# Kernel tuning notes

Hardware: AMD Instinct MI355X
Metric: run time of the kernel (lower is better)

The kernel has to match this reference:

```python
import jax, jax.numpy as jnp
import numpy as np

TEMP = 0.5
NUM_QUERIES = 256
NUM_NEGATIVES = 256
STRONG_THRESHOLD = 0.97


def _l2norm(x):
    n = jnp.sqrt(jnp.sum(x * x, axis=-1, keepdims=True))
    return x / jnp.maximum(n, 1e-12)


def _mls(mu0, mu1, s0, s1, w0, w1):
    # mutual likelihood score, mean over feature dim
    mu0 = _l2norm(mu0)
    mu1 = _l2norm(mu1)
    up = (mu0 * w0 - mu1 * w1) ** 2
    down = s0 * w0 + s1 * w1
    return -0.5 * jnp.mean(up / down + jnp.log(down), axis=-1)


def setup_inputs() -> dict:
    key = jax.random.key(0)
    B, C, H, W, S = 4, 32, 256, 256, 8
    ks = jax.random.split(key, 6)
    weights = jax.random.uniform(ks[0], (B, C, H, W), jnp.float32, 0.1, 1.0)
    mu = jax.random.normal(ks[1], (B, C, H, W), jnp.float32)
    sigma = jax.random.uniform(ks[2], (B, C, H, W), jnp.float32, 0.1, 1.0)
    cls = jax.random.randint(ks[3], (B, H, W), 0, S)
    label = jax.nn.one_hot(cls, S, axis=1, dtype=jnp.float32)  # [B,S,H,W]
    mask = (jax.random.uniform(ks[4], (B, 1, H, W)) < 0.7).astype(jnp.float32)
    prob = jax.random.uniform(ks[5], (B, S, H, W), jnp.float32)
    return {"weights": weights, "mu": mu, "sigma": sigma, "label": label, "mask": mask, "prob": prob}


def _rank_table(m, N):
    # m: bool [S, N]. table[s, r] = pixel index with rank r within class s.
    S = m.shape[0]
    ranks = jnp.cumsum(m, axis=1) - 1
    idx = jnp.where(m, ranks, N)  # out-of-range entries are dropped
    tbl = jnp.zeros((S, N), jnp.int32)
    rows = jnp.broadcast_to(jnp.arange(S)[:, None], (S, N))
    vals = jnp.broadcast_to(jnp.arange(N, dtype=jnp.int32)[None, :], (S, N))
    return tbl.at[rows, idx].set(vals, mode="drop")


def _forward(weights, mu, sigma, label, mask, prob):
    B, C, H, W = mu.shape
    S = label.shape[1]
    N = B * H * W
    Q, NEG = NUM_QUERIES, NUM_NEGATIVES
    mu_f = jnp.transpose(mu, (0, 2, 3, 1)).reshape(N, C)
    sig_f = jnp.transpose(sigma, (0, 2, 3, 1)).reshape(N, C)
    w_f = jnp.transpose(weights, (0, 2, 3, 1)).reshape(N, C)
    valid = jnp.transpose(label * mask, (1, 0, 2, 3)).reshape(S, N)  # [S,N]
    prob_f = jnp.transpose(prob, (1, 0, 2, 3)).reshape(S, N)
    vmask = valid > 0
    hmask = vmask & (prob_f < STRONG_THRESHOLD)
    count = jnp.sum(vmask, axis=1)
    hcount = jnp.sum(hmask, axis=1)
    # prototypes: masked sums over valid pixels (no_grad in original)
    inv_sig_w = w_f / sig_f
    proto_sigma = 1.0 / (valid @ inv_sig_w)                    # [S,C]
    proto_mu = proto_sigma * (valid @ (inv_sig_w * mu_f))      # [S,C]
    proto_weight = 1.0 / (valid @ (1.0 / w_f))                 # [S,C]
    proto_mu, proto_sigma, proto_weight = map(jax.lax.stop_gradient, (proto_mu, proto_sigma, proto_weight))
    tbl_valid = _rank_table(vmask, N)
    tbl_hard = _rank_table(hmask, N)
    keys = jax.random.split(jax.random.key(42), S)

    def per_class(i, key):
        k1, k2, k3 = jax.random.split(key, 3)
        # anchor sampling from hard pixels of class i (differentiable gather)
        ra = jnp.minimum((jax.random.uniform(k1, (Q,)) * hcount[i]).astype(jnp.int32), jnp.maximum(hcount[i] - 1, 0))
        apix = tbl_hard[i, ra]
        a_mu, a_sig, a_w = mu_f[apix], sig_f[apix], w_f[apix]
        # negative class distribution from prototype similarity
        order = (i + 1 + jnp.arange(S - 1)) % S
        sim = _mls(proto_mu[i][None], proto_mu[order], proto_sigma[i][None], proto_sigma[order], proto_weight[i][None], proto_weight[order])
        sim = jnp.where(count[order] > 0, sim, -jnp.inf)
        cls_pick = jax.random.categorical(k2, sim / TEMP, shape=(Q, NEG))
        neg_cls = order[cls_pick]                              # [Q,NEG]
        cnt = count[neg_cls]
        rn = jnp.minimum((jax.random.uniform(k3, (Q, NEG)) * cnt).astype(jnp.int32), jnp.maximum(cnt - 1, 0))
        npix = tbl_valid[neg_cls, rn]                          # [Q,NEG]
        n_mu = jax.lax.stop_gradient(mu_f[npix])
        n_sig = jax.lax.stop_gradient(sig_f[npix])
        n_w = jax.lax.stop_gradient(w_f[npix])
        pos_mu = jnp.broadcast_to(proto_mu[i], (Q, 1, C))
        pos_sig = jnp.broadcast_to(proto_sigma[i], (Q, 1, C))
        pos_w = jnp.broadcast_to(proto_weight[i], (Q, 1, C))
        all_mu = jnp.concatenate([pos_mu, n_mu], axis=1)       # [Q,1+NEG,C]
        all_sig = jnp.concatenate([pos_sig, n_sig], axis=1)
        all_w = jnp.concatenate([pos_w, n_w], axis=1)
        logits = _mls(a_mu[:, None], all_mu, a_sig[:, None], all_sig, a_w[:, None], all_w) / TEMP
        ce = jnp.mean(jax.nn.logsumexp(logits, axis=1) - logits[:, 0])
        ok = (hcount[i] > 0) & (count[i] > 0)
        return jnp.where(ok, ce, 0.0)

    losses = jax.vmap(per_class)(jnp.arange(S), keys)
    valid_num = jnp.sum(count > 0)
    return jnp.sum(losses) / valid_num.astype(losses.dtype)


def reference(weights, mu, sigma, label, mask, prob):
    return _forward(weights, mu, sigma, label, mask, prob)
```

## Files before the change

### kernel.cpp

```cpp
#include <hip/hip_runtime.h>
#include <hip/hip_fp16.h>
#include <stdint.h>


#define NPIX  262144
#define NCLS  8
#define NQ    256
#define NNEG  256
#define NE    257
#define NBLK  1024

typedef unsigned short u16;
typedef unsigned int   u32;

struct TFKeys { u32 k1[8][2], k2[8][2], k3[8][2]; };

__host__ __device__ inline void tf2x32(u32 k0, u32 k1, u32 x0, u32 x1, u32& o0, u32& o1) {
  u32 ks2 = k0 ^ k1 ^ 0x1BD11BDAu;
  x0 += k0; x1 += k1;
#define TFR(R) { x0 += x1; x1 = (x1 << (R)) | (x1 >> (32 - (R))); x1 ^= x0; }
  TFR(13) TFR(15) TFR(26) TFR(6)
  x0 += k1;  x1 += ks2 + 1u;
  TFR(17) TFR(29) TFR(16) TFR(24)
  x0 += ks2; x1 += k0 + 2u;
  TFR(13) TFR(15) TFR(26) TFR(6)
  x0 += k0;  x1 += k1 + 3u;
  TFR(17) TFR(29) TFR(16) TFR(24)
  x0 += k1;  x1 += ks2 + 4u;
  TFR(13) TFR(15) TFR(26) TFR(6)
  x0 += ks2; x1 += k0 + 5u;
#undef TFR
  o0 = x0; o1 = x1;
}

__device__ inline float bfv(u16 v) { return __uint_as_float(((u32)v) << 16); }
__device__ inline float lo16(u32 v) { return __uint_as_float(v << 16); }
__device__ inline float hi16(u32 v) { return __uint_as_float(v & 0xFFFF0000u); }
__device__ inline float u01(u32 bits) { return __uint_as_float((bits >> 9) | 0x3F800000u) - 1.0f; }
__device__ inline u32 rbits(u32 k0, u32 k1, u32 idx) { u32 a, b; tf2x32(k0, k1, 0u, idx, a, b); return a ^ b; }
__device__ inline u32 packPQ(float p, float q) {
  return (u32)__half_as_ushort(__float2half(p)) | ((u32)__half_as_ushort(__float2half(q)) << 16);
}
__device__ inline float2 unpackPQ(u32 v) {
  return make_float2(__half2float(__ushort_as_half((u16)(v & 0xFFFFu))),
                     __half2float(__ushort_as_half((u16)(v >> 16))));
}

__global__ __launch_bounds__(256) void k_flags(const u16* __restrict__ lab, const u16* __restrict__ msk,
                                               const u16* __restrict__ prb, unsigned char* __restrict__ flags,
                                               int* __restrict__ blockCnt,
                                               float* __restrict__ protoAcc, float* __restrict__ ceAcc,
                                               int* __restrict__ diag) {
  __shared__ int cnt[16];
  int tid = threadIdx.x;
  if (blockIdx.x == 0) {
    for (int i = tid; i < 768; i += 256) protoAcc[i] = 0.f;
    if (tid < 8) ceAcc[tid] = 0.f;
    if (tid == 0) diag[0] = 0;
  }
  if (tid < 16) cnt[tid] = 0;
  __syncthreads();
  int n = blockIdx.x * 256 + tid;
  int b = n >> 16, hw = n & 65535;
  float m = bfv(msk[(b << 16) + hw]);
  int cls = 0; bool v = false;
  for (int s = 0; s < 8; s++) {
    float l = bfv(lab[((size_t)(b * 8 + s) << 16) + hw]);
    if (l * m > 0.f) { cls = s; v = true; }
  }
  bool h = false;
  if (v) { float p = bfv(prb[((size_t)(b * 8 + cls) << 16) + hw]); h = p < 0.97f; }
  flags[n] = (unsigned char)(cls | (v ? 16 : 0) | (h ? 32 : 0));
  if (v) atomicAdd(&cnt[cls], 1);
  if (h) atomicAdd(&cnt[8 + cls], 1);
  __syncthreads();
  if (tid < 16) blockCnt[tid * NBLK + blockIdx.x] = cnt[tid];
}

__global__ __launch_bounds__(1024) void k_scan(const int* __restrict__ blockCnt, int* __restrict__ blockOff,
                                               int* __restrict__ counts) {
  int ctr = threadIdx.x >> 6, lane = threadIdx.x & 63;
  int run = 0;
  for (int ch = 0; ch < 16; ch++) {
    int bidx = ch * 64 + lane;
    int v = blockCnt[ctr * NBLK + bidx];
    int x = v;
    for (int d = 1; d < 64; d <<= 1) { int t = __shfl_up(x, d); if (lane >= d) x += t; }
    blockOff[ctr * NBLK + bidx] = run + x - v;
    run += __shfl(x, 63);
  }
  if (lane == 0) counts[ctr] = run;
}

__global__ __launch_bounds__(256) void k_place(const unsigned char* __restrict__ flags, const int* __restrict__ blockOff,
                                               int* __restrict__ tblV, int* __restrict__ tblH) {
  __shared__ int wcnt[4][16];
  int tid = threadIdx.x;
  int n = blockIdx.x * 256 + tid;
  int f = flags[n];
  int cls = f & 15; bool v = (f & 16) != 0, h = (f & 32) != 0;
  int wave = tid >> 6, lane = tid & 63;
  unsigned long long below = (1ull << lane) - 1ull;
  int rv = 0, rh = 0;
  for (int s = 0; s < 8; s++) {
    unsigned long long bv = __ballot(v && (cls == s));
    unsigned long long bh = __ballot(h && (cls == s));
    if (lane == 0) { wcnt[wave][s] = __popcll(bv); wcnt[wave][8 + s] = __popcll(bh); }
    if (cls == s) { rv = __popcll(bv & below); rh = __popcll(bh & below); }
  }
  __syncthreads();
  int preV = 0, preH = 0;
  for (int w2 = 0; w2 < wave; w2++) { preV += wcnt[w2][cls]; preH += wcnt[w2][8 + cls]; }
  if (v) tblV[(size_t)cls * NPIX + blockOff[cls * NBLK + blockIdx.x] + preV + rv] = n;
  if (h) tblH[(size_t)cls * NPIX + blockOff[(8 + cls) * NBLK + blockIdx.x] + preH + rh] = n;
}

__global__ __launch_bounds__(256) void k_pq(const u16* __restrict__ mu, const u16* __restrict__ wgt,
                                            const u16* __restrict__ sig, u32* __restrict__ PQ) {
  __shared__ u32 tile[256 * 33];
  int t = threadIdx.x;
  int n0 = blockIdx.x * 512;
  int b = n0 >> 16;
  int hwt = (n0 & 65535) + 2 * t;
  size_t cb = ((size_t)(b * 32)) << 16;
  u32 m2[32];
  float ss0 = 0.f, ss1 = 0.f;
  #pragma unroll
  for (int c = 0; c < 32; c++) {
    m2[c] = *(const u32*)(mu + cb + ((size_t)c << 16) + hwt);
    float a = lo16(m2[c]), d = hi16(m2[c]);
    ss0 += a * a; ss1 += d * d;
  }
  float rn0 = 1.0f / fmaxf(sqrtf(ss0), 1e-12f);
  float rn1 = 1.0f / fmaxf(sqrtf(ss1), 1e-12f);
  u32 pk0[32], pk1[32];
  #pragma unroll
  for (int c = 0; c < 32; c++) {
    u32 w2 = *(const u32*)(wgt + cb + ((size_t)c << 16) + hwt);
    u32 s2 = *(const u32*)(sig + cb + ((size_t)c << 16) + hwt);
    pk0[c] = packPQ(lo16(m2[c]) * rn0 * lo16(w2), lo16(s2) * lo16(w2));
    pk1[c] = packPQ(hi16(m2[c]) * rn1 * hi16(w2), hi16(s2) * hi16(w2));
  }
  #pragma unroll
  for (int ch = 0; ch < 2; ch++) {
    if ((t >> 7) == ch) {
      int l = t & 127;
      #pragma unroll
      for (int c = 0; c < 32; c++) {
        tile[(2 * l + 0) * 33 + c] = pk0[c];
        tile[(2 * l + 1) * 33 + c] = pk1[c];
      }
    }
    __syncthreads();
    uint4* dst = (uint4*)(PQ + (size_t)(n0 + ch * 256) * 32);
    for (int k = t; k < 2048; k += 256) {
      int p = k >> 3, c4 = (k & 7) * 4;
      dst[k] = make_uint4(tile[p * 33 + c4], tile[p * 33 + c4 + 1],
                          tile[p * 33 + c4 + 2], tile[p * 33 + c4 + 3]);
    }
    __syncthreads();
  }
}

__global__ __launch_bounds__(256) void k_proto(const u16* __restrict__ mu, const u16* __restrict__ wgt,
                                               const u16* __restrict__ sig, const int* __restrict__ tblV,
                                               const int* __restrict__ counts, float* __restrict__ protoAcc) {
  int ch = blockIdx.x & 7;
  int s  = (blockIdx.x >> 3) & 7;
  int c  = blockIdx.x >> 6;
  int sc = s * 32 + c;
  int cnt = counts[s];
  const int* row = tblV + (size_t)s * NPIX;
  float a0 = 0.f, a1 = 0.f, a2 = 0.f;
  int r = ch * 256 + threadIdx.x;
  for (; r + 6144 < cnt; r += 8192) {
    int p0 = row[r], p1 = row[r + 2048], p2 = row[r + 4096], p3 = row[r + 6144];
    size_t A0 = (((size_t)((p0 >> 16) * 32 + c)) << 16) + (p0 & 65535);
    size_t A1 = (((size_t)((p1 >> 16) * 32 + c)) << 16) + (p1 & 65535);
    size_t A2 = (((size_t)((p2 >> 16) * 32 + c)) << 16) + (p2 & 65535);
    size_t A3 = (((size_t)((p3 >> 16) * 32 + c)) << 16) + (p3 & 65535);
    float m0 = bfv(mu[A0]), w0 = bfv(wgt[A0]), s0 = bfv(sig[A0]);
    float m1 = bfv(mu[A1]), w1 = bfv(wgt[A1]), s1 = bfv(sig[A1]);
    float m2_ = bfv(mu[A2]), w2 = bfv(wgt[A2]), s2 = bfv(sig[A2]);
    float m3 = bfv(mu[A3]), w3 = bfv(wgt[A3]), s3 = bfv(sig[A3]);
    float i0 = w0 / s0, i1 = w1 / s1, i2 = w2 / s2, i3 = w3 / s3;
    a0 += i0; a1 += i0 * m0; a2 += 1.0f / w0;
    a0 += i1; a1 += i1 * m1; a2 += 1.0f / w1;
    a0 += i2; a1 += i2 * m2_; a2 += 1.0f / w2;
    a0 += i3; a1 += i3 * m3; a2 += 1.0f / w3;
  }
  for (; r < cnt; r += 2048) {
    int pix = row[r];
    size_t a = (((size_t)((pix >> 16) * 32 + c)) << 16) + (pix & 65535);
    float mv = bfv(mu[a]), wv = bfv(wgt[a]), sv = bfv(sig[a]);
    float isw = wv / sv;
    a0 += isw; a1 += isw * mv; a2 += 1.0f / wv;
  }
  #pragma unroll
  for (int d = 1; d < 64; d <<= 1) {
    a0 += __shfl_xor(a0, d);
    a1 += __shfl_xor(a1, d);
    a2 += __shfl_xor(a2, d);
  }
  if ((threadIdx.x & 63) == 0) {
    atomicAdd(&protoAcc[sc * 3 + 0], a0);
    atomicAdd(&protoAcc[sc * 3 + 1], a1);
    atomicAdd(&protoAcc[sc * 3 + 2], a2);
  }
}

__global__ void k_protoFinal(const float* __restrict__ protoAcc, const int* __restrict__ counts,
                             u32* __restrict__ protoPQ, float* __restrict__ simL,
                             int* __restrict__ diag) {
  __shared__ float sP[256], sQ[256];
  __shared__ int alive;
  int tid = threadIdx.x;
  if (tid == 0) alive = 0;
  float a0 = protoAcc[tid * 3 + 0], a1 = protoAcc[tid * 3 + 1], a2 = protoAcc[tid * 3 + 2];
  bool have = counts[tid >> 5] > 0;
  bool ok = (a0 > 0.f) && (a2 > 0.f);
  __syncthreads();
  if (have && !ok) atomicOr(diag, 2);
  if (have && ok) alive = 1;
  float psig = 1.0f / a0;
  float pmu  = psig * a1;
  float pw   = 1.0f / a2;
  float sq = (have && ok) ? pmu * pmu : 0.f;
  #pragma unroll
  for (int d = 1; d < 32; d <<= 1) sq += __shfl_xor(sq, d);
  float rn = 1.0f / fmaxf(sqrtf(sq), 1e-12f);
  float pP = (have && ok) ? pmu * rn * pw : 0.f;
  float pQ = (have && ok) ? psig * pw : 0.f;
  sP[tid] = pP; sQ[tid] = pQ;
  protoPQ[tid] = packPQ(pP, pQ);
  __syncthreads();
  if (tid == 0 && alive == 0) atomicOr(diag, 32);
  if (tid < 64) {
    int i = tid >> 3, j = tid & 7;
    if (j < 7) {
      int o = (i + 1 + j) & 7;
      float acc = 0.f;
      for (int c = 0; c < 32; c++) {
        float d = sP[i * 32 + c] - sP[o * 32 + c];
        float dn = sQ[i * 32 + c] + sQ[o * 32 + c];
        acc += d * d / dn + logf(dn);
      }
      float sim = -0.5f * (acc * (1.0f / 32.0f));
      simL[i * 8 + j] = (counts[o] > 0) ? (sim * 2.0f) : -INFINITY;
    }
  }
}

__global__ __launch_bounds__(256) void k_sample(TFKeys K, const float* __restrict__ simL,
                                                const int* __restrict__ counts,
                                                const int* __restrict__ tblV, const int* __restrict__ tblH,
                                                const u32* __restrict__ PQ, const u32* __restrict__ protoPQ,
                                                float* __restrict__ ceAcc, int* __restrict__ diag) {
  __shared__ __align__(16) u32 sA[32];
  __shared__ float redM[4], redS[4];
  __shared__ int sAp;
  int blk = blockIdx.x;
  int i = blk >> 8, q = blk & 255;
  int t = threadIdx.x;
  if (t == 0) {
    u32 bits = rbits(K.k1[i][0], K.k1[i][1], (u32)q);
    float u = u01(bits);
    int hc = counts[8 + i];
    int ra = (int)(u * (float)hc);
    int cap = hc - 1; if (cap < 0) cap = 0;
    if (ra > cap) ra = cap; if (ra < 0) ra = 0;
    int p = tblH[(size_t)i * NPIX + ra];
    if (p < 0) p = 0; if (p > NPIX - 1) p = NPIX - 1;
    sAp = p;
  }
  __syncthreads();
  if (t < 32) sA[t] = PQ[(size_t)sAp * 32 + t];
  u32 rem = (u32)(q * 256 + t);
  u32 k20 = K.k2[i][0], k21 = K.k2[i][1];
  float Lr[7];
  #pragma unroll
  for (int j = 0; j < 7; j++) Lr[j] = simL[i * 8 + j];
  float mg = 0.f; int pick = 0;
  #pragma unroll
  for (int j = 0; j < 7; j++) {
    u32 bits = rbits(k20, k21, rem * 7u + (u32)j);
    float f = u01(bits);
    float u = fmaxf(f, 1.17549435e-38f);
    float g = -logf(-logf(u));
    float v = g + Lr[j];
    if (j == 0) { mg = v; } else if (v > mg) { mg = v; pick = j; }
  }
  int nc = (i + 1 + pick) & 7;
  u32 bits3 = rbits(K.k3[i][0], K.k3[i][1], rem);
  float u3 = u01(bits3);
  int cntv = counts[nc];
  int rn = (int)(u3 * (float)cntv);
  int cap2 = cntv - 1; if (cap2 < 0) cap2 = 0;
  if (rn > cap2) rn = cap2; if (rn < 0) rn = 0;
  int np = tblV[(size_t)nc * NPIX + rn];
  if (np < 0) np = 0; if (np > NPIX - 1) np = NPIX - 1;
  __syncthreads();
  const uint4* A4 = (const uint4*)sA;
  const uint4* B  = (const uint4*)(PQ + (size_t)np * 32);
  float accN = 0.f;
  #pragma unroll
  for (int k = 0; k < 8; k++) {
    uint4 ua = A4[k], ub = B[k];
    float2 fa, fb; float d, dn;
    fa = unpackPQ(ua.x); fb = unpackPQ(ub.x); d = fa.x - fb.x; dn = fa.y + fb.y; accN += d * d / dn + __logf(dn);
    fa = unpackPQ(ua.y); fb = unpackPQ(ub.y); d = fa.x - fb.x; dn = fa.y + fb.y; accN += d * d / dn + __logf(dn);
    fa = unpackPQ(ua.z); fb = unpackPQ(ub.z); d = fa.x - fb.x; dn = fa.y + fb.y; accN += d * d / dn + __logf(dn);
    fa = unpackPQ(ua.w); fb = unpackPQ(ub.w); d = fa.x - fb.x; dn = fa.y + fb.y; accN += d * d / dn + __logf(dn);
  }
  float lN = -(accN * (1.0f / 32.0f));
  float l0 = 0.f;
  if (t == 0) {
    const uint4* B0 = (const uint4*)(protoPQ + i * 32);
    float acc0 = 0.f;
    #pragma unroll
    for (int k = 0; k < 8; k++) {
      uint4 ua = A4[k], ub = B0[k];
      float2 fa, fb; float d, dn;
      fa = unpackPQ(ua.x); fb = unpackPQ(ub.x); d = fa.x - fb.x; dn = fa.y + fb.y; acc0 += d * d / dn + __logf(dn);
      fa = unpackPQ(ua.y); fb = unpackPQ(ub.y); d = fa.x - fb.x; dn = fa.y + fb.y; acc0 += d * d / dn + __logf(dn);
      fa = unpackPQ(ua.z); fb = unpackPQ(ub.z); d = fa.x - fb.x; dn = fa.y + fb.y; acc0 += d * d / dn + __logf(dn);
      fa = unpackPQ(ua.w); fb = unpackPQ(ub.w); d = fa.x - fb.x; dn = fa.y + fb.y; acc0 += d * d / dn + __logf(dn);
    }
    l0 = -(acc0 * (1.0f / 32.0f));
  }
  bool bad = !(lN == lN) || (t == 0 && !(l0 == l0));
  if (__ballot(bad) != 0ull && (t & 63) == 0) atomicOr(diag, 8);
  float lm = (t == 0) ? fmaxf(lN, l0) : lN;
  #pragma unroll
  for (int d = 1; d < 64; d <<= 1) lm = fmaxf(lm, __shfl_xor(lm, d));
  if ((t & 63) == 0) redM[t >> 6] = lm;
  __syncthreads();
  float M = fmaxf(fmaxf(redM[0], redM[1]), fmaxf(redM[2], redM[3]));
  float es = __expf(lN - M) + ((t == 0) ? __expf(l0 - M) : 0.f);
  #pragma unroll
  for (int d = 1; d < 64; d <<= 1) es += __shfl_xor(es, d);
  if ((t & 63) == 0) redS[t >> 6] = es;
  __syncthreads();
  if (t == 0) {
    float S = redS[0] + redS[1] + redS[2] + redS[3];
    float ce = (M + __logf(S)) - l0;
    atomicAdd(&ceAcc[i], ce);
  }
}

__global__ void k_final(const float* __restrict__ ceAcc, const int* __restrict__ counts,
                        const int* __restrict__ diag, u32* __restrict__ out) {
  if (blockIdx.x == 0 && threadIdx.x == 0) {
    float loss = 0.f; int vn = 0;
    int db = diag[0];
    for (int i = 0; i < 8; i++) {
      if (counts[i] > 0) vn++;
      float ce = ceAcc[i];
      if (counts[i] > 0 && counts[8 + i] > 0) {
        if (!(ce == ce)) db |= 4;
        loss += ce * (1.0f / 256.0f);
      }
    }
    if (vn == 0) db |= 1;
    loss = loss / (float)vn;
    if (!(loss == loss) && db == 0) db = 16;
    if (db != 0) loss = 4096.0f * (float)(1 + db);
    u32 fb = __float_as_uint(loss);
    u32 bv = (fb + 0x7FFFu + ((fb >> 16) & 1u)) >> 16;
    out[0] = (fb & 0xFFFF0000u) | (bv & 0xFFFFu);
  }
}

extern "C" void kernel_launch(void* const* d_in, const int* in_sizes, int n_in,
                              void* d_out, int out_size, void* d_ws, size_t ws_size,
                              hipStream_t stream) {
  (void)in_sizes; (void)n_in; (void)out_size; (void)ws_size;
  const u16* wgt = (const u16*)d_in[0];
  const u16* mu  = (const u16*)d_in[1];
  const u16* sig = (const u16*)d_in[2];
  const u16* lab = (const u16*)d_in[3];
  const u16* msk = (const u16*)d_in[4];
  const u16* prb = (const u16*)d_in[5];

  char* wp = (char*)d_ws;
  auto take = [&](size_t bytes) -> void* { void* p = (void*)wp; wp += ((bytes + 255) & ~(size_t)255); return p; };
  u32*   PQ       = (u32*)  take((size_t)NPIX * 32 * 4);
  int*   tblV     = (int*)  take((size_t)NCLS * NPIX * 4);
  int*   tblH     = (int*)  take((size_t)NCLS * NPIX * 4);
  unsigned char* flags = (unsigned char*)take(NPIX);
  int*   blockCnt = (int*)  take(16 * NBLK * 4);
  int*   blockOff = (int*)  take(16 * NBLK * 4);
  float* protoAcc = (float*)take(768 * 4);
  u32*   protoPQ  = (u32*)  take(256 * 4);
  float* simL     = (float*)take(64 * 4);
  int*   counts   = (int*)  take(16 * 4);
  float* ceAcc    = (float*)take(8 * 4);
  int*   diag     = (int*)  take(4);

  TFKeys K;
  for (u32 i = 0; i < 8; i++) {
    u32 ki0, ki1;
    tf2x32(0u, 42u, 0u, i, ki0, ki1);
    tf2x32(ki0, ki1, 0u, 0u, K.k1[i][0], K.k1[i][1]);
    tf2x32(ki0, ki1, 0u, 1u, K.k2[i][0], K.k2[i][1]);
    tf2x32(ki0, ki1, 0u, 2u, K.k3[i][0], K.k3[i][1]);
  }

  k_flags<<<1024, 256, 0, stream>>>(lab, msk, prb, flags, blockCnt, protoAcc, ceAcc, diag);
  k_scan<<<1, 1024, 0, stream>>>(blockCnt, blockOff, counts);
  k_place<<<1024, 256, 0, stream>>>(flags, blockOff, tblV, tblH);
  k_pq<<<512, 256, 0, stream>>>(mu, wgt, sig, PQ);
  k_proto<<<2048, 256, 0, stream>>>(mu, wgt, sig, tblV, counts, protoAcc);
  k_protoFinal<<<1, 256, 0, stream>>>(protoAcc, counts, protoPQ, simL, diag);
  k_sample<<<2048, 256, 0, stream>>>(K, simL, counts, tblV, tblH, PQ, protoPQ, ceAcc, diag);
  k_final<<<1, 64, 0, stream>>>(ceAcc, counts, diag, (u32*)d_out);
}
```

Measured before the change: 232.5 us.

## Fold scan, protoFinal and final kernels into neighbors via last-block counters

Removes three tiny single-block launches by merging the block-count scan into an extra block of k_pq, and the prototype finalization and loss reduction into the last finishing block of k_proto and k_sample via atomic counters. k_flags now processes four pixels per thread with vectorized loads, emitting four sub-block counts per block. The MLS inner loop replaces per-element log with products of denominators and two logs, plus fast division, cutting transcendental work. Risks: the product of 16 denominators could overflow or underflow, and the scan block in k_pq sits at the tail of the grid.

```diff
diff --git a/kernel.cpp b/kernel.cpp
--- a/kernel.cpp
+++ b/kernel.cpp
@@ -7,7 +7,6 @@
 #define NCLS  8
 #define NQ    256
 #define NNEG  256
-#define NE    257
 #define NBLK  1024
 
 typedef unsigned short u16;
@@ -45,51 +44,119 @@
   return make_float2(__half2float(__ushort_as_half((u16)(v & 0xFFFFu))),
                      __half2float(__ushort_as_half((u16)(v >> 16))));
 }
+__device__ inline float aload(const float* p) {
+  return __hip_atomic_load(p, __ATOMIC_RELAXED, __HIP_MEMORY_SCOPE_AGENT);
+}
 
 __global__ __launch_bounds__(256) void k_flags(const u16* __restrict__ lab, const u16* __restrict__ msk,
                                                const u16* __restrict__ prb, unsigned char* __restrict__ flags,
                                                int* __restrict__ blockCnt,
                                                float* __restrict__ protoAcc, float* __restrict__ ceAcc,
-                                               int* __restrict__ diag) {
-  __shared__ int cnt[16];
-  int tid = threadIdx.x;
+                                               int* __restrict__ diag, int* __restrict__ syncCtr) {
+  __shared__ int cnt[4][16];
+  int t = threadIdx.x;
   if (blockIdx.x == 0) {
-    for (int i = tid; i < 768; i += 256) protoAcc[i] = 0.f;
-    if (tid < 8) ceAcc[tid] = 0.f;
-    if (tid == 0) diag[0] = 0;
-  }
-  if (tid < 16) cnt[tid] = 0;
-  __syncthreads();
-  int n = blockIdx.x * 256 + tid;
-  int b = n >> 16, hw = n & 65535;
-  float m = bfv(msk[(b << 16) + hw]);
-  int cls = 0; bool v = false;
+    for (int i = t; i < 768; i += 256) protoAcc[i] = 0.f;
+    if (t < 8) ceAcc[t] = 0.f;
+    if (t == 0) { diag[0] = 0; syncCtr[0] = 0; syncCtr[1] = 0; }
+  }
+  if (t < 64) cnt[t >> 4][t & 15] = 0;
+  __syncthreads();
+  int n0 = blockIdx.x * 1024;
+  int b = n0 >> 16;
+  int hwt = (n0 & 65535) + 4 * t;
+  uint2 mr = *(const uint2*)(msk + ((size_t)b << 16) + hwt);
+  float m[4] = { lo16(mr.x), hi16(mr.x), lo16(mr.y), hi16(mr.y) };
+  int cls[4] = {0, 0, 0, 0};
+  bool v[4] = {false, false, false, false};
+  #pragma unroll
   for (int s = 0; s < 8; s++) {
-    float l = bfv(lab[((size_t)(b * 8 + s) << 16) + hw]);
-    if (l * m > 0.f) { cls = s; v = true; }
-  }
-  bool h = false;
-  if (v) { float p = bfv(prb[((size_t)(b * 8 + cls) << 16) + hw]); h = p < 0.97f; }
-  flags[n] = (unsigned char)(cls | (v ? 16 : 0) | (h ? 32 : 0));
-  if (v) atomicAdd(&cnt[cls], 1);
-  if (h) atomicAdd(&cnt[8 + cls], 1);
-  __syncthreads();
-  if (tid < 16) blockCnt[tid * NBLK + blockIdx.x] = cnt[tid];
-}
-
-__global__ __launch_bounds__(1024) void k_scan(const int* __restrict__ blockCnt, int* __restrict__ blockOff,
-                                               int* __restrict__ counts) {
-  int ctr = threadIdx.x >> 6, lane = threadIdx.x & 63;
-  int run = 0;
-  for (int ch = 0; ch < 16; ch++) {
-    int bidx = ch * 64 + lane;
-    int v = blockCnt[ctr * NBLK + bidx];
-    int x = v;
-    for (int d = 1; d < 64; d <<= 1) { int t = __shfl_up(x, d); if (lane >= d) x += t; }
-    blockOff[ctr * NBLK + bidx] = run + x - v;
-    run += __shfl(x, 63);
-  }
-  if (lane == 0) counts[ctr] = run;
+    uint2 lr = *(const uint2*)(lab + (((size_t)(b * 8 + s)) << 16) + hwt);
+    float l[4] = { lo16(lr.x), hi16(lr.x), lo16(lr.y), hi16(lr.y) };
+    #pragma unroll
+    for (int j = 0; j < 4; j++) if (l[j] * m[j] > 0.f) { cls[j] = s; v[j] = true; }
+  }
+  int qtr = t >> 6;
+  u32 fw = 0;
+  #pragma unroll
+  for (int j = 0; j < 4; j++) {
+    bool h = false;
+    if (v[j]) { float p = bfv(prb[(((size_t)(b * 8 + cls[j])) << 16) + hwt + j]); h = p < 0.97f; }
+    int f = cls[j] | (v[j] ? 16 : 0) | (h ? 32 : 0);
+    fw |= ((u32)f) << (8 * j);
+    if (v[j]) atomicAdd(&cnt[qtr][cls[j]], 1);
+    if (h)    atomicAdd(&cnt[qtr][8 + cls[j]], 1);
+  }
+  *(u32*)(flags + n0 + 4 * t) = fw;
+  __syncthreads();
+  if (t < 64) blockCnt[(t & 15) * NBLK + blockIdx.x * 4 + (t >> 4)] = cnt[t >> 4][t & 15];
+}
+
+__global__ __launch_bounds__(256) void k_pq(const u16* __restrict__ mu, const u16* __restrict__ wgt,
+                                            const u16* __restrict__ sig, u32* __restrict__ PQ,
+                                            const int* __restrict__ blockCnt, int* __restrict__ blockOff,
+                                            int* __restrict__ counts) {
+  if (blockIdx.x == 512) {
+    int t = threadIdx.x;
+    int w = t >> 6, lane = t & 63;
+    for (int cc = 0; cc < 4; cc++) {
+      int ctr = w * 4 + cc;
+      int run = 0;
+      for (int chk = 0; chk < 16; chk++) {
+        int bidx = chk * 64 + lane;
+        int v = blockCnt[ctr * NBLK + bidx];
+        int x = v;
+        for (int d = 1; d < 64; d <<= 1) { int tt = __shfl_up(x, d); if (lane >= d) x += tt; }
+        blockOff[ctr * NBLK + bidx] = run + x - v;
+        run += __shfl(x, 63);
+      }
+      if (lane == 0) counts[ctr] = run;
+    }
+    return;
+  }
+  __shared__ u32 tile[256 * 33];
+  int t = threadIdx.x;
+  int n0 = blockIdx.x * 512;
+  int b = n0 >> 16;
+  int hwt = (n0 & 65535) + 2 * t;
+  size_t cb = ((size_t)(b * 32)) << 16;
+  u32 m2[32];
+  float ss0 = 0.f, ss1 = 0.f;
+  #pragma unroll
+  for (int c = 0; c < 32; c++) {
+    m2[c] = *(const u32*)(mu + cb + ((size_t)c << 16) + hwt);
+    float a = lo16(m2[c]), d = hi16(m2[c]);
+    ss0 += a * a; ss1 += d * d;
+  }
+  float rn0 = 1.0f / fmaxf(sqrtf(ss0), 1e-12f);
+  float rn1 = 1.0f / fmaxf(sqrtf(ss1), 1e-12f);
+  u32 pk0[32], pk1[32];
+  #pragma unroll
+  for (int c = 0; c < 32; c++) {
+    u32 w2 = *(const u32*)(wgt + cb + ((size_t)c << 16) + hwt);
+    u32 s2 = *(const u32*)(sig + cb + ((size_t)c << 16) + hwt);
+    pk0[c] = packPQ(lo16(m2[c]) * rn0 * lo16(w2), lo16(s2) * lo16(w2));
+    pk1[c] = packPQ(hi16(m2[c]) * rn1 * hi16(w2), hi16(s2) * hi16(w2));
+  }
+  #pragma unroll
+  for (int ch = 0; ch < 2; ch++) {
+    if ((t >> 7) == ch) {
+      int l = t & 127;
+      #pragma unroll
+      for (int c = 0; c < 32; c++) {
+        tile[(2 * l + 0) * 33 + c] = pk0[c];
+        tile[(2 * l + 1) * 33 + c] = pk1[c];
+      }
+    }
+    __syncthreads();
+    uint4* dst = (uint4*)(PQ + (size_t)(n0 + ch * 256) * 32);
+    for (int k = t; k < 2048; k += 256) {
+      int p = k >> 3, c4 = (k & 7) * 4;
+      dst[k] = make_uint4(tile[p * 33 + c4], tile[p * 33 + c4 + 1],
+                          tile[p * 33 + c4 + 2], tile[p * 33 + c4 + 3]);
+    }
+    __syncthreads();
+  }
 }
 
 __global__ __launch_bounds__(256) void k_place(const unsigned char* __restrict__ flags, const int* __restrict__ blockOff,
@@ -115,56 +182,11 @@
   if (h) tblH[(size_t)cls * NPIX + blockOff[(8 + cls) * NBLK + blockIdx.x] + preH + rh] = n;
 }
 
-__global__ __launch_bounds__(256) void k_pq(const u16* __restrict__ mu, const u16* __restrict__ wgt,
-                                            const u16* __restrict__ sig, u32* __restrict__ PQ) {
-  __shared__ u32 tile[256 * 33];
-  int t = threadIdx.x;
-  int n0 = blockIdx.x * 512;
-  int b = n0 >> 16;
-  int hwt = (n0 & 65535) + 2 * t;
-  size_t cb = ((size_t)(b * 32)) << 16;
-  u32 m2[32];
-  float ss0 = 0.f, ss1 = 0.f;
-  #pragma unroll
-  for (int c = 0; c < 32; c++) {
-    m2[c] = *(const u32*)(mu + cb + ((size_t)c << 16) + hwt);
-    float a = lo16(m2[c]), d = hi16(m2[c]);
-    ss0 += a * a; ss1 += d * d;
-  }
-  float rn0 = 1.0f / fmaxf(sqrtf(ss0), 1e-12f);
-  float rn1 = 1.0f / fmaxf(sqrtf(ss1), 1e-12f);
-  u32 pk0[32], pk1[32];
-  #pragma unroll
-  for (int c = 0; c < 32; c++) {
-    u32 w2 = *(const u32*)(wgt + cb + ((size_t)c << 16) + hwt);
-    u32 s2 = *(const u32*)(sig + cb + ((size_t)c << 16) + hwt);
-    pk0[c] = packPQ(lo16(m2[c]) * rn0 * lo16(w2), lo16(s2) * lo16(w2));
-    pk1[c] = packPQ(hi16(m2[c]) * rn1 * hi16(w2), hi16(s2) * hi16(w2));
-  }
-  #pragma unroll
-  for (int ch = 0; ch < 2; ch++) {
-    if ((t >> 7) == ch) {
-      int l = t & 127;
-      #pragma unroll
-      for (int c = 0; c < 32; c++) {
-        tile[(2 * l + 0) * 33 + c] = pk0[c];
-        tile[(2 * l + 1) * 33 + c] = pk1[c];
-      }
-    }
-    __syncthreads();
-    uint4* dst = (uint4*)(PQ + (size_t)(n0 + ch * 256) * 32);
-    for (int k = t; k < 2048; k += 256) {
-      int p = k >> 3, c4 = (k & 7) * 4;
-      dst[k] = make_uint4(tile[p * 33 + c4], tile[p * 33 + c4 + 1],
-                          tile[p * 33 + c4 + 2], tile[p * 33 + c4 + 3]);
-    }
-    __syncthreads();
-  }
-}
-
 __global__ __launch_bounds__(256) void k_proto(const u16* __restrict__ mu, const u16* __restrict__ wgt,
                                                const u16* __restrict__ sig, const int* __restrict__ tblV,
-                                               const int* __restrict__ counts, float* __restrict__ protoAcc) {
+                                               const int* __restrict__ counts, float* __restrict__ protoAcc,
+                                               u32* __restrict__ protoPQ, float* __restrict__ simL,
+                                               int* __restrict__ diag, int* __restrict__ syncCtr) {
   int ch = blockIdx.x & 7;
   int s  = (blockIdx.x >> 3) & 7;
   int c  = blockIdx.x >> 6;
@@ -207,24 +229,29 @@
     atomicAdd(&protoAcc[sc * 3 + 1], a1);
     atomicAdd(&protoAcc[sc * 3 + 2], a2);
   }
-}
-
-__global__ void k_protoFinal(const float* __restrict__ protoAcc, const int* __restrict__ counts,
-                             u32* __restrict__ protoPQ, float* __restrict__ simL,
-                             int* __restrict__ diag) {
+  __shared__ int sLast;
+  __syncthreads();
+  if (threadIdx.x == 0) {
+    __threadfence();
+    sLast = (atomicAdd(&syncCtr[0], 1) == 2047) ? 1 : 0;
+  }
+  __syncthreads();
+  if (!sLast) return;
   __shared__ float sP[256], sQ[256];
   __shared__ int alive;
   int tid = threadIdx.x;
   if (tid == 0) alive = 0;
-  float a0 = protoAcc[tid * 3 + 0], a1 = protoAcc[tid * 3 + 1], a2 = protoAcc[tid * 3 + 2];
+  float b0 = aload(&protoAcc[tid * 3 + 0]);
+  float b1 = aload(&protoAcc[tid * 3 + 1]);
+  float b2 = aload(&protoAcc[tid * 3 + 2]);
   bool have = counts[tid >> 5] > 0;
-  bool ok = (a0 > 0.f) && (a2 > 0.f);
+  bool ok = (b0 > 0.f) && (b2 > 0.f);
   __syncthreads();
   if (have && !ok) atomicOr(diag, 2);
   if (have && ok) alive = 1;
-  float psig = 1.0f / a0;
-  float pmu  = psig * a1;
-  float pw   = 1.0f / a2;
+  float psig = 1.0f / b0;
+  float pmu  = psig * b1;
+  float pw   = 1.0f / b2;
   float sq = (have && ok) ? pmu * pmu : 0.f;
   #pragma unroll
   for (int d = 1; d < 32; d <<= 1) sq += __shfl_xor(sq, d);
@@ -240,9 +267,9 @@
     if (j < 7) {
       int o = (i + 1 + j) & 7;
       float acc = 0.f;
-      for (int c = 0; c < 32; c++) {
-        float d = sP[i * 32 + c] - sP[o * 32 + c];
-        float dn = sQ[i * 32 + c] + sQ[o * 32 + c];
+      for (int cc = 0; cc < 32; cc++) {
+        float d = sP[i * 32 + cc] - sP[o * 32 + cc];
+        float dn = sQ[i * 32 + cc] + sQ[o * 32 + cc];
         acc += d * d / dn + logf(dn);
       }
       float sim = -0.5f * (acc * (1.0f / 32.0f));
@@ -255,7 +282,8 @@
                                                 const int* __restrict__ counts,
                                                 const int* __restrict__ tblV, const int* __restrict__ tblH,
                                                 const u32* __restrict__ PQ, const u32* __restrict__ protoPQ,
-                                                float* __restrict__ ceAcc, int* __restrict__ diag) {
+                                                float* __restrict__ ceAcc, int* __restrict__ diag,
+                                                int* __restrict__ syncCtr, u32* __restrict__ out) {
   __shared__ __align__(16) u32 sA[32];
   __shared__ float redM[4], redS[4];
   __shared__ int sAp;
@@ -286,7 +314,7 @@
     u32 bits = rbits(k20, k21, rem * 7u + (u32)j);
     float f = u01(bits);
     float u = fmaxf(f, 1.17549435e-38f);
-    float g = -logf(-logf(u));
+    float g = -__logf(-__logf(u));
     float v = g + Lr[j];
     if (j == 0) { mg = v; } else if (v > mg) { mg = v; pick = j; }
   }
@@ -302,31 +330,31 @@
   __syncthreads();
   const uint4* A4 = (const uint4*)sA;
   const uint4* B  = (const uint4*)(PQ + (size_t)np * 32);
-  float accN = 0.f;
+  float accD = 0.f, pr0 = 1.f, pr1 = 1.f;
   #pragma unroll
   for (int k = 0; k < 8; k++) {
     uint4 ua = A4[k], ub = B[k];
     float2 fa, fb; float d, dn;
-    fa = unpackPQ(ua.x); fb = unpackPQ(ub.x); d = fa.x - fb.x; dn = fa.y + fb.y; accN += d * d / dn + __logf(dn);
-    fa = unpackPQ(ua.y); fb = unpackPQ(ub.y); d = fa.x - fb.x; dn = fa.y + fb.y; accN += d * d / dn + __logf(dn);
-    fa = unpackPQ(ua.z); fb = unpackPQ(ub.z); d = fa.x - fb.x; dn = fa.y + fb.y; accN += d * d / dn + __logf(dn);
-    fa = unpackPQ(ua.w); fb = unpackPQ(ub.w); d = fa.x - fb.x; dn = fa.y + fb.y; accN += d * d / dn + __logf(dn);
-  }
-  float lN = -(accN * (1.0f / 32.0f));
+    fa = unpackPQ(ua.x); fb = unpackPQ(ub.x); d = fa.x - fb.x; dn = fa.y + fb.y; accD += __fdividef(d * d, dn); if (k < 4) pr0 *= dn; else pr1 *= dn;
+    fa = unpackPQ(ua.y); fb = unpackPQ(ub.y); d = fa.x - fb.x; dn = fa.y + fb.y; accD += __fdividef(d * d, dn); if (k < 4) pr0 *= dn; else pr1 *= dn;
+    fa = unpackPQ(ua.z); fb = unpackPQ(ub.z); d = fa.x - fb.x; dn = fa.y + fb.y; accD += __fdividef(d * d, dn); if (k < 4) pr0 *= dn; else pr1 *= dn;
+    fa = unpackPQ(ua.w); fb = unpackPQ(ub.w); d = fa.x - fb.x; dn = fa.y + fb.y; accD += __fdividef(d * d, dn); if (k < 4) pr0 *= dn; else pr1 *= dn;
+  }
+  float lN = -((accD + __logf(pr0) + __logf(pr1)) * (1.0f / 32.0f));
   float l0 = 0.f;
   if (t == 0) {
     const uint4* B0 = (const uint4*)(protoPQ + i * 32);
-    float acc0 = 0.f;
+    float aD = 0.f, p0_ = 1.f, p1_ = 1.f;
     #pragma unroll
     for (int k = 0; k < 8; k++) {
       uint4 ua = A4[k], ub = B0[k];
       float2 fa, fb; float d, dn;
-      fa = unpackPQ(ua.x); fb = unpackPQ(ub.x); d = fa.x - fb.x; dn = fa.y + fb.y; acc0 += d * d / dn + __logf(dn);
-      fa = unpackPQ(ua.y); fb = unpackPQ(ub.y); d = fa.x - fb.x; dn = fa.y + fb.y; acc0 += d * d / dn + __logf(dn);
-      fa = unpackPQ(ua.z); fb = unpackPQ(ub.z); d = fa.x - fb.x; dn = fa.y + fb.y; acc0 += d * d / dn + __logf(dn);
-      fa = unpackPQ(ua.w); fb = unpackPQ(ub.w); d = fa.x - fb.x; dn = fa.y + fb.y; acc0 += d * d / dn + __logf(dn);
-    }
-    l0 = -(acc0 * (1.0f / 32.0f));
+      fa = unpackPQ(ua.x); fb = unpackPQ(ub.x); d = fa.x - fb.x; dn = fa.y + fb.y; aD += __fdividef(d * d, dn); if (k < 4) p0_ *= dn; else p1_ *= dn;
+      fa = unpackPQ(ua.y); fb = unpackPQ(ub.y); d = fa.x - fb.x; dn = fa.y + fb.y; aD += __fdividef(d * d, dn); if (k < 4) p0_ *= dn; else p1_ *= dn;
+      fa = unpackPQ(ua.z); fb = unpackPQ(ub.z); d = fa.x - fb.x; dn = fa.y + fb.y; aD += __fdividef(d * d, dn); if (k < 4) p0_ *= dn; else p1_ *= dn;
+      fa = unpackPQ(ua.w); fb = unpackPQ(ub.w); d = fa.x - fb.x; dn = fa.y + fb.y; aD += __fdividef(d * d, dn); if (k < 4) p0_ *= dn; else p1_ *= dn;
+    }
+    l0 = -((aD + __logf(p0_) + __logf(p1_)) * (1.0f / 32.0f));
   }
   bool bad = !(lN == lN) || (t == 0 && !(l0 == l0));
   if (__ballot(bad) != 0ull && (t & 63) == 0) atomicOr(diag, 8);
@@ -346,17 +374,20 @@
     float ce = (M + __logf(S)) - l0;
     atomicAdd(&ceAcc[i], ce);
   }
-}
-
-__global__ void k_final(const float* __restrict__ ceAcc, const int* __restrict__ counts,
-                        const int* __restrict__ diag, u32* __restrict__ out) {
-  if (blockIdx.x == 0 && threadIdx.x == 0) {
+  __shared__ int sLast;
+  __syncthreads();
+  if (t == 0) {
+    __threadfence();
+    sLast = (atomicAdd(&syncCtr[1], 1) == 2047) ? 1 : 0;
+  }
+  __syncthreads();
+  if (sLast && t == 0) {
     float loss = 0.f; int vn = 0;
-    int db = diag[0];
-    for (int i = 0; i < 8; i++) {
-      if (counts[i] > 0) vn++;
-      float ce = ceAcc[i];
-      if (counts[i] > 0 && counts[8 + i] > 0) {
+    int db = __hip_atomic_load(diag, __ATOMIC_RELAXED, __HIP_MEMORY_SCOPE_AGENT);
+    for (int ii = 0; ii < 8; ii++) {
+      if (counts[ii] > 0) vn++;
+      float ce = aload(&ceAcc[ii]);
+      if (counts[ii] > 0 && counts[8 + ii] > 0) {
         if (!(ce == ce)) db |= 4;
         loss += ce * (1.0f / 256.0f);
       }
@@ -396,6 +427,7 @@
   int*   counts   = (int*)  take(16 * 4);
   float* ceAcc    = (float*)take(8 * 4);
   int*   diag     = (int*)  take(4);
+  int*   syncCtr  = (int*)  take(8);
 
   TFKeys K;
   for (u32 i = 0; i < 8; i++) {
@@ -406,12 +438,9 @@
     tf2x32(ki0, ki1, 0u, 2u, K.k3[i][0], K.k3[i][1]);
   }
 
-  k_flags<<<1024, 256, 0, stream>>>(lab, msk, prb, flags, blockCnt, protoAcc, ceAcc, diag);
-  k_scan<<<1, 1024, 0, stream>>>(blockCnt, blockOff, counts);
+  k_flags<<<256, 256, 0, stream>>>(lab, msk, prb, flags, blockCnt, protoAcc, ceAcc, diag, syncCtr);
+  k_pq<<<513, 256, 0, stream>>>(mu, wgt, sig, PQ, blockCnt, blockOff, counts);
   k_place<<<1024, 256, 0, stream>>>(flags, blockOff, tblV, tblH);
-  k_pq<<<512, 256, 0, stream>>>(mu, wgt, sig, PQ);
-  k_proto<<<2048, 256, 0, stream>>>(mu, wgt, sig, tblV, counts, protoAcc);
-  k_protoFinal<<<1, 256, 0, stream>>>(protoAcc, counts, protoPQ, simL, diag);
-  k_sample<<<2048, 256, 0, stream>>>(K, simL, counts, tblV, tblH, PQ, protoPQ, ceAcc, diag);
-  k_final<<<1, 64, 0, stream>>>(ceAcc, counts, diag, (u32*)d_out);
-}
+  k_proto<<<2048, 256, 0, stream>>>(mu, wgt, sig, tblV, counts, protoAcc, protoPQ, simL, diag, syncCtr);
+  k_sample<<<2048, 256, 0, stream>>>(K, simL, counts, tblV, tblH, PQ, protoPQ, ceAcc, diag, syncCtr, (u32*)d_out);
+}
```

Result: slower. 322.3 us (+38.6%).
